# Performance work log

Measured on AMD Instinct MI355X. Metric: run time of the kernel, lower is better.

## Reference

```python
import jax, jax.numpy as jnp
import numpy as np

C = 64  # num_channels
B, H, W = 16, 160, 160


def squeeze2d(x, f=2):
    b, c, h, w = x.shape
    x = x.reshape(b, c, h // f, f, w // f, f)
    x = x.transpose(0, 1, 3, 5, 2, 4)
    return x.reshape(b, c * f * f, h // f, w // f)


def unsqueeze2d(x, f=2):
    b, c, h, w = x.shape
    x = x.reshape(b, c // (f * f), f, f, h, w)
    x = x.transpose(0, 1, 4, 2, 5, 3)
    return x.reshape(b, c // (f * f), h * f, w * f)


def get_indices(num_channels):
    # generate_ind(p) tiles the row-major-flattened 2x2 pattern over C//4 channel groups
    def gen(p):
        return np.tile(np.array(p, dtype=bool), num_channels // 4)
    m = np.ones(num_channels, dtype=bool)
    t = gen([0, 0, 1, 1]); b = ~t
    l = gen([0, 1, 0, 1]); r = ~l
    return (m, t, b, l, r, t & l, t & r, b & l, b & r)


INDS = get_indices(C)


def conv1x1(z, w):
    # 1x1 conv == channel matmul
    return jnp.einsum('oc,bchw->bohw', w, z)


def partition_input(x):
    z = unsqueeze2d(x)
    z = jnp.pad(z, ((0, 0), (0, 0), (1, 1), (1, 1)), constant_values=-1.0)
    z = squeeze2d(z)  # (B, C, H+1, W+1)
    m, t, b, l, r, tl, tr, bl, br = INDS
    return (z[:, :, 1:-1, 1:-1],
            z[:, t, :1, 1:-1], z[:, b, -1:, 1:-1],
            z[:, l, 1:-1, :1], z[:, r, 1:-1, -1:],
            z[:, tl, :1, :1], z[:, tr, :1, -1:],
            z[:, bl, -1:, :1], z[:, br, -1:, -1:])


def unsqueeze_line(ze):
    b, c = ze.shape[:2]
    sz = (1, -1) if ze.shape[-2] == 1 else (-1, 1)
    return ze.reshape(b, c // 2, 2, -1).transpose(0, 1, 3, 2).reshape(b, c // 2, *sz)


def merge_output(z_m, z_t, z_b, z_l, z_r, z_tl, z_tr, z_bl, z_br):
    z_m = unsqueeze2d(z_m)
    z_t, z_b, z_l, z_r = [unsqueeze_line(zi) for zi in (z_t, z_b, z_l, z_r)]
    z_tt = jnp.concatenate([z_tl, z_t, z_tr], axis=3)
    z_mm = jnp.concatenate([z_l, z_m, z_r], axis=3)
    z_bb = jnp.concatenate([z_bl, z_b, z_br], axis=3)
    return squeeze2d(jnp.concatenate([z_tt, z_mm, z_bb], axis=2))


def setup_inputs() -> dict:
    key = jax.random.key(0)
    k1, k2 = jax.random.split(key)
    x = jax.random.normal(k1, (B, C, H, W), dtype=jnp.float32)
    logdet = jax.random.normal(k2, (B,), dtype=jnp.float32)
    rng = np.random.RandomState(0)
    w_init = np.linalg.qr(rng.randn(C, C))[0].astype(np.float32)
    weight = jnp.asarray(w_init)
    return {"input": x, "logdet": logdet, "weight": weight}


def reference(input, logdet, weight):
    h, w = input.shape[-2:]
    pixels = [(h - 1) * (w - 1), w - 1, w - 1, h - 1, h - 1, 1, 1, 1, 1]
    ws = [weight[np.ix_(ind, ind)] for ind in INDS]
    dlogdet = sum(jnp.linalg.slogdet(wi)[1] * p for wi, p in zip(ws, pixels))
    zs = partition_input(input)
    outs = [conv1x1(z, wi) for z, wi in zip(zs, ws)]
    output = merge_output(*outs)
    return output, logdet + dlogdet
```

## Files before the change

kernel.cpp:

```cpp
#include <hip/hip_runtime.h>
#include <math.h>

#define NB 16
#define NC 64
#define HW 160
#define PLANE (HW * HW)
#define SG 161
#define SGSQ (SG * SG)
#define NSITES (NB * SGSQ)
#define OUT_LD_OFF (NB * NC * PLANE)
#define TILE 256
#define NCONV ((NSITES + TILE - 1) / TILE)

#define SMEM_FLOATS 9476

__device__ inline int chmap(int i, int n, int pa, int pb) {
    if (n == 64) return i;
    if (n == 32) return ((i >> 1) << 2) | ((i & 1) ? pb : pa);
    return (i << 2) | pa;
}

template <int N>
__device__ float group_lu_logabsdet(const float* __restrict__ W, float* A,
                                    int pa, int pb, int lane) {
    const int r = lane & (N - 1);
    constexpr int LD = N + 1;
#pragma unroll 4
    for (int i = 0; i < N; ++i)
        A[i * LD + r] = W[chmap(i, N, pa, pb) * 64 + chmap(r, N, pa, pb)];
    asm volatile("s_waitcnt lgkmcnt(0) vmcnt(0)" ::: "memory");
    float logdet = 0.f;
    for (int k = 0; k < N; ++k) {
        float cand = (r >= k) ? fabsf(A[r * LD + k]) : -1.f;
        int idx = r;
#pragma unroll
        for (int off = N >> 1; off; off >>= 1) {
            float oc = __shfl_xor(cand, off, N);
            int oi = __shfl_xor(idx, off, N);
            if (oc > cand || (oc == cand && oi < idx)) { cand = oc; idx = oi; }
        }
        const int p = idx;
        if (p != k) {
            float tk = A[k * LD + r];
            float tp = A[p * LD + r];
            A[k * LD + r] = tp;
            A[p * LD + r] = tk;
        }
        asm volatile("s_waitcnt lgkmcnt(0)" ::: "memory");
        float piv = A[k * LD + k];
        logdet += logf(fabsf(piv));
        float rpiv = 1.f / piv;
        if (r > k) {
            float wk = A[k * LD + r] * rpiv;
            int i = k + 1;
            for (; i + 3 < N; i += 4) {
                float a0 = A[(i + 0) * LD + k], a1 = A[(i + 1) * LD + k],
                      a2 = A[(i + 2) * LD + k], a3 = A[(i + 3) * LD + k];
                float x0 = A[(i + 0) * LD + r], x1 = A[(i + 1) * LD + r],
                      x2 = A[(i + 2) * LD + r], x3 = A[(i + 3) * LD + r];
                A[(i + 0) * LD + r] = fmaf(-a0, wk, x0);
                A[(i + 1) * LD + r] = fmaf(-a1, wk, x1);
                A[(i + 2) * LD + r] = fmaf(-a2, wk, x2);
                A[(i + 3) * LD + r] = fmaf(-a3, wk, x3);
            }
            for (; i < N; ++i) {
                float a0 = A[i * LD + k], x0 = A[i * LD + r];
                A[i * LD + r] = fmaf(-a0, wk, x0);
            }
        }
        asm volatile("s_waitcnt lgkmcnt(0)" ::: "memory");
    }
    return logdet;
}

__global__ __launch_bounds__(256, 4) void InvConv1x1GridAlign_kernel(
    const float* __restrict__ x, const float* __restrict__ ld_in,
    const float* __restrict__ W, float* __restrict__ out) {
    __shared__ __align__(16) float smem[SMEM_FLOATS];
    const int tid = threadIdx.x;

    if (blockIdx.x == 0) {
        float* A64 = smem;
        float* A32a = smem + 4160;
        float* A32b = smem + 6272;
        float* A16 = smem + 8384;
        float* partial = smem + 9472;
        int wid = tid >> 6;
        int lane = tid & 63;
        float part = 0.f;
        if (wid == 0) {
            part = 25281.f * group_lu_logabsdet<64>(W, A64, 0, 0, lane);
        } else if (wid == 1) {
            int g = lane >> 5;
            float ld = group_lu_logabsdet<32>(W, A32a + g * (32 * 33),
                                              g ? 0 : 2, g ? 1 : 3, lane);
            part = (__shfl(ld, 0, 64) + __shfl(ld, 32, 64)) * 159.f;
        } else if (wid == 2) {
            int g = lane >> 5;
            float ld = group_lu_logabsdet<32>(W, A32b + g * (32 * 33),
                                              g ? 0 : 1, g ? 2 : 3, lane);
            part = (__shfl(ld, 0, 64) + __shfl(ld, 32, 64)) * 159.f;
        } else {
            int g = lane >> 4;
            float ld = group_lu_logabsdet<16>(W, A16 + g * (16 * 17),
                                              3 - g, 0, lane);
            part = __shfl(ld, 0, 64) + __shfl(ld, 16, 64) +
                   __shfl(ld, 32, 64) + __shfl(ld, 48, 64);
        }
        if (lane == 0) partial[wid] = part;
        __syncthreads();
        if (tid < NB) {
            float dl = partial[0] + partial[1] + partial[2] + partial[3];
            out[OUT_LD_OFF + tid] = ld_in[tid] + dl;
        }
        return;
    }

    const int tile0 = ((int)blockIdx.x - 1) * TILE;
    const int lane = tid & 63;
    const int wid = tid >> 6;
    const int wo = __builtin_amdgcn_readfirstlane(wid << 4);

    const int offm[4] = {0, 1, HW, HW + 1};
    bool vm[4];
    int baseoff;
    const float* xb;
    {
        int s = tile0 + tid;
        bool sok = s < NSITES;
        unsigned us = (unsigned)(sok ? s : 0);
        unsigned b = us / SGSQ;
        unsigned rr = us - b * SGSQ;
        unsigned Y = rr / SG;
        unsigned X = rr - Y * SG;
        xb = x + (size_t)b * (NC * PLANE);
        baseoff = ((int)Y - 1) * HW + ((int)X - 1);
        bool okT = sok && (Y >= 1), okB = sok && (Y <= HW - 1);
        bool okL = (X >= 1), okR = (X <= HW - 1);
        vm[0] = okT && okL; vm[1] = okT && okR;
        vm[2] = okB && okL; vm[3] = okB && okR;
    }

    float acc[16][4];
#pragma unroll
    for (int j = 0; j < 16; ++j)
#pragma unroll
        for (int s2 = 0; s2 < 4; ++s2) acc[j][s2] = 0.f;

#pragma unroll 1
    for (int half = 0; half < 2; ++half) {
        __syncthreads();
#pragma unroll 8
        for (int krow = 0; krow < 32; ++krow) {
            const int k = (half << 5) + krow;
            const int pl = k ^ 3;
            const int m = krow & 3;
            float val = vm[m] ? xb[pl * PLANE + baseoff + offm[m]] : 0.f;
            smem[(krow << 8) + tid] = val;
        }
        __syncthreads();
#pragma unroll 1
        for (int kb = 0; kb < 8; ++kb) {
            float v[4][4];
            const float* vb = smem + (kb << 10) + lane;
#pragma unroll
            for (int kk = 0; kk < 4; ++kk)
#pragma unroll
                for (int s2 = 0; s2 < 4; ++s2)
                    v[kk][s2] = vb[(kk << 8) + (s2 << 6)];
            const int k0 = (half << 5) + (kb << 2);
#pragma unroll
            for (int jb = 0; jb < 2; ++jb) {
                float4 w4[8];
#pragma unroll
                for (int j = 0; j < 8; ++j)
                    w4[j] = *(const float4*)(W + (wo + (jb << 3) + j) * 64 + k0);
#pragma unroll
                for (int j = 0; j < 8; ++j) {
                    const int jj = (jb << 3) + j;
#pragma unroll
                    for (int kk = 0; kk < 4; ++kk) {
                        const float wjk = (kk == 0) ? w4[j].x
                                        : (kk == 1) ? w4[j].y
                                        : (kk == 2) ? w4[j].z : w4[j].w;
#pragma unroll
                        for (int s2 = 0; s2 < 4; ++s2)
                            acc[jj][s2] = fmaf(wjk, v[kk][s2], acc[jj][s2]);
                    }
                }
            }
        }
    }

#pragma unroll
    for (int s2 = 0; s2 < 4; ++s2) {
        int s = tile0 + lane + (s2 << 6);
        bool sok = s < NSITES;
        unsigned us = (unsigned)(sok ? s : 0);
        unsigned b = us / SGSQ;
        unsigned rr = us - b * SGSQ;
        unsigned Y = rr / SG;
        unsigned X = rr - Y * SG;
        float* ob = out + (size_t)b * (NC * PLANE);
        int boff = ((int)Y - 1) * HW + ((int)X - 1);
        bool okT = sok && (Y >= 1), okB = sok && (Y <= HW - 1);
        bool okL = (X >= 1), okR = (X <= HW - 1);
        bool wm[4] = {okT && okL, okT && okR, okB && okL, okB && okR};
#pragma unroll
        for (int j = 0; j < 16; ++j) {
            const int o = wo + j;
            const int pl = o ^ 3;
            const int m = j & 3;
            if (wm[m]) ob[pl * PLANE + boff + offm[m]] = acc[j][s2];
        }
    }
}

extern "C" void kernel_launch(void* const* d_in, const int* in_sizes, int n_in,
                              void* d_out, int out_size, void* d_ws, size_t ws_size,
                              hipStream_t stream) {
    const float* x = (const float*)d_in[0];
    const float* ld = (const float*)d_in[1];
    const float* W = (const float*)d_in[2];
    float* out = (float*)d_out;
    hipLaunchKernelGGL(InvConv1x1GridAlign_kernel, dim3(NCONV + 1), dim3(256), 0,
                       stream, x, ld, W, out);
}
```

Measured before the change: 252.5 us.

## Split determinant into separate kernel and register-tile conv without shared memory

Moves the LU log-determinant work into its own single-block kernel launched after the main conv kernel. The main kernel now has each thread own one site and compute 32 of the 64 output channels, using two blocks per tile. Inputs are loaded straight from global memory into registers with double-buffered 16-channel chunks and masked by multiplication instead of staged through LDS. This drops shared memory and barriers, but each input is now read twice (once per output half), there is a second launch, and register pressure rises.

```diff
diff --git a/kernel.cpp b/kernel.cpp
--- a/kernel.cpp
+++ b/kernel.cpp
@@ -12,7 +12,7 @@
 #define TILE 256
 #define NCONV ((NSITES + TILE - 1) / TILE)
 
-#define SMEM_FLOATS 9476
+#define DET_SMEM_FLOATS 9476
 
 __device__ inline int chmap(int i, int n, int pa, int pb) {
     if (n == 64) return i;
@@ -73,60 +73,91 @@
     return logdet;
 }
 
-__global__ __launch_bounds__(256, 4) void InvConv1x1GridAlign_kernel(
-    const float* __restrict__ x, const float* __restrict__ ld_in,
-    const float* __restrict__ W, float* __restrict__ out) {
-    __shared__ __align__(16) float smem[SMEM_FLOATS];
+__global__ __launch_bounds__(256, 4) void InvConvDet_kernel(
+    const float* __restrict__ ld_in, const float* __restrict__ W,
+    float* __restrict__ out) {
+    __shared__ __align__(16) float smem[DET_SMEM_FLOATS];
     const int tid = threadIdx.x;
-
-    if (blockIdx.x == 0) {
-        float* A64 = smem;
-        float* A32a = smem + 4160;
-        float* A32b = smem + 6272;
-        float* A16 = smem + 8384;
-        float* partial = smem + 9472;
-        int wid = tid >> 6;
-        int lane = tid & 63;
-        float part = 0.f;
-        if (wid == 0) {
-            part = 25281.f * group_lu_logabsdet<64>(W, A64, 0, 0, lane);
-        } else if (wid == 1) {
-            int g = lane >> 5;
-            float ld = group_lu_logabsdet<32>(W, A32a + g * (32 * 33),
-                                              g ? 0 : 2, g ? 1 : 3, lane);
-            part = (__shfl(ld, 0, 64) + __shfl(ld, 32, 64)) * 159.f;
-        } else if (wid == 2) {
-            int g = lane >> 5;
-            float ld = group_lu_logabsdet<32>(W, A32b + g * (32 * 33),
-                                              g ? 0 : 1, g ? 2 : 3, lane);
-            part = (__shfl(ld, 0, 64) + __shfl(ld, 32, 64)) * 159.f;
-        } else {
-            int g = lane >> 4;
-            float ld = group_lu_logabsdet<16>(W, A16 + g * (16 * 17),
-                                              3 - g, 0, lane);
-            part = __shfl(ld, 0, 64) + __shfl(ld, 16, 64) +
-                   __shfl(ld, 32, 64) + __shfl(ld, 48, 64);
-        }
-        if (lane == 0) partial[wid] = part;
-        __syncthreads();
-        if (tid < NB) {
-            float dl = partial[0] + partial[1] + partial[2] + partial[3];
-            out[OUT_LD_OFF + tid] = ld_in[tid] + dl;
-        }
-        return;
-    }
-
-    const int tile0 = ((int)blockIdx.x - 1) * TILE;
-    const int lane = tid & 63;
-    const int wid = tid >> 6;
-    const int wo = __builtin_amdgcn_readfirstlane(wid << 4);
+    float* A64 = smem;
+    float* A32a = smem + 4160;
+    float* A32b = smem + 6272;
+    float* A16 = smem + 8384;
+    float* partial = smem + 9472;
+    int wid = tid >> 6;
+    int lane = tid & 63;
+    float part = 0.f;
+    if (wid == 0) {
+        part = 25281.f * group_lu_logabsdet<64>(W, A64, 0, 0, lane);
+    } else if (wid == 1) {
+        int g = lane >> 5;
+        float ld = group_lu_logabsdet<32>(W, A32a + g * (32 * 33),
+                                          g ? 0 : 2, g ? 1 : 3, lane);
+        part = (__shfl(ld, 0, 64) + __shfl(ld, 32, 64)) * 159.f;
+    } else if (wid == 2) {
+        int g = lane >> 5;
+        float ld = group_lu_logabsdet<32>(W, A32b + g * (32 * 33),
+                                          g ? 0 : 1, g ? 2 : 3, lane);
+        part = (__shfl(ld, 0, 64) + __shfl(ld, 32, 64)) * 159.f;
+    } else {
+        int g = lane >> 4;
+        float ld = group_lu_logabsdet<16>(W, A16 + g * (16 * 17), 3 - g, 0, lane);
+        part = __shfl(ld, 0, 64) + __shfl(ld, 16, 64) +
+               __shfl(ld, 32, 64) + __shfl(ld, 48, 64);
+    }
+    if (lane == 0) partial[wid] = part;
+    __syncthreads();
+    if (tid < NB) {
+        float dl = partial[0] + partial[1] + partial[2] + partial[3];
+        out[OUT_LD_OFF + tid] = ld_in[tid] + dl;
+    }
+}
+
+
+#define LOADCH(dst, cc)                                                      \
+    {                                                                        \
+        _Pragma("unroll") for (int i = 0; i < 16; ++i)                       \
+            dst[i] = xb[(size_t)(((cc) << 4) + (i ^ 3)) * PLANE +            \
+                        aoff[i & 3]];                                        \
+    }
+
+#define COMPCH(src, cc)                                                      \
+    {                                                                        \
+        _Pragma("unroll") for (int i = 0; i < 16; ++i) src[i] *= mf[i & 3];  \
+        _Pragma("unroll") for (int j = 0; j < 32; ++j) {                     \
+            const float* wr = wbase + j * 64 + ((cc) << 4);                  \
+            float4 w0 = *(const float4*)(wr + 0);                            \
+            float4 w1 = *(const float4*)(wr + 4);                            \
+            float4 w2 = *(const float4*)(wr + 8);                            \
+            float4 w3 = *(const float4*)(wr + 12);                           \
+            float a = u[j];                                                  \
+            a = fmaf(w0.x, src[0], a);  a = fmaf(w0.y, src[1], a);           \
+            a = fmaf(w0.z, src[2], a);  a = fmaf(w0.w, src[3], a);           \
+            a = fmaf(w1.x, src[4], a);  a = fmaf(w1.y, src[5], a);           \
+            a = fmaf(w1.z, src[6], a);  a = fmaf(w1.w, src[7], a);           \
+            a = fmaf(w2.x, src[8], a);  a = fmaf(w2.y, src[9], a);           \
+            a = fmaf(w2.z, src[10], a); a = fmaf(w2.w, src[11], a);          \
+            a = fmaf(w3.x, src[12], a); a = fmaf(w3.y, src[13], a);          \
+            a = fmaf(w3.z, src[14], a); a = fmaf(w3.w, src[15], a);          \
+            u[j] = a;                                                        \
+        }                                                                    \
+    }
+
+__global__ __launch_bounds__(256, 5) void InvConvMain_kernel(
+    const float* __restrict__ x, const float* __restrict__ W,
+    float* __restrict__ out) {
+    const int tid = threadIdx.x;
+    const int bid = blockIdx.x;
+    const int ohalf = bid & 1;
+    const int s = (bid >> 1) * TILE + tid;
 
     const int offm[4] = {0, 1, HW, HW + 1};
     bool vm[4];
+    int aoff[4];
+    float mf[4];
     int baseoff;
     const float* xb;
+    float* ob;
     {
-        int s = tile0 + tid;
         bool sok = s < NSITES;
         unsigned us = (unsigned)(sok ? s : 0);
         unsigned b = us / SGSQ;
@@ -134,84 +165,44 @@
         unsigned Y = rr / SG;
         unsigned X = rr - Y * SG;
         xb = x + (size_t)b * (NC * PLANE);
+        ob = out + (size_t)b * (NC * PLANE);
         baseoff = ((int)Y - 1) * HW + ((int)X - 1);
         bool okT = sok && (Y >= 1), okB = sok && (Y <= HW - 1);
         bool okL = (X >= 1), okR = (X <= HW - 1);
         vm[0] = okT && okL; vm[1] = okT && okR;
         vm[2] = okB && okL; vm[3] = okB && okR;
-    }
-
-    float acc[16][4];
-#pragma unroll
-    for (int j = 0; j < 16; ++j)
-#pragma unroll
-        for (int s2 = 0; s2 < 4; ++s2) acc[j][s2] = 0.f;
-
-#pragma unroll 1
-    for (int half = 0; half < 2; ++half) {
-        __syncthreads();
-#pragma unroll 8
-        for (int krow = 0; krow < 32; ++krow) {
-            const int k = (half << 5) + krow;
-            const int pl = k ^ 3;
-            const int m = krow & 3;
-            float val = vm[m] ? xb[pl * PLANE + baseoff + offm[m]] : 0.f;
-            smem[(krow << 8) + tid] = val;
-        }
-        __syncthreads();
-#pragma unroll 1
-        for (int kb = 0; kb < 8; ++kb) {
-            float v[4][4];
-            const float* vb = smem + (kb << 10) + lane;
-#pragma unroll
-            for (int kk = 0; kk < 4; ++kk)
-#pragma unroll
-                for (int s2 = 0; s2 < 4; ++s2)
-                    v[kk][s2] = vb[(kk << 8) + (s2 << 6)];
-            const int k0 = (half << 5) + (kb << 2);
-#pragma unroll
-            for (int jb = 0; jb < 2; ++jb) {
-                float4 w4[8];
-#pragma unroll
-                for (int j = 0; j < 8; ++j)
-                    w4[j] = *(const float4*)(W + (wo + (jb << 3) + j) * 64 + k0);
-#pragma unroll
-                for (int j = 0; j < 8; ++j) {
-                    const int jj = (jb << 3) + j;
-#pragma unroll
-                    for (int kk = 0; kk < 4; ++kk) {
-                        const float wjk = (kk == 0) ? w4[j].x
-                                        : (kk == 1) ? w4[j].y
-                                        : (kk == 2) ? w4[j].z : w4[j].w;
-#pragma unroll
-                        for (int s2 = 0; s2 < 4; ++s2)
-                            acc[jj][s2] = fmaf(wjk, v[kk][s2], acc[jj][s2]);
-                    }
-                }
+#pragma unroll
+        for (int m = 0; m < 4; ++m) {
+            aoff[m] = vm[m] ? (baseoff + offm[m]) : 0;
+            mf[m] = vm[m] ? 1.f : 0.f;
+        }
+    }
+
+    const float* wbase = W + (ohalf << 5) * 64;
+
+    float u[32];
+#pragma unroll
+    for (int j = 0; j < 32; ++j) u[j] = 0.f;
+
+    float va[16], vb[16];
+    LOADCH(va, 0)
+    LOADCH(vb, 1)
+    COMPCH(va, 0)
+    LOADCH(va, 2)
+    COMPCH(vb, 1)
+    LOADCH(vb, 3)
+    COMPCH(va, 2)
+    COMPCH(vb, 3)
+
+#pragma unroll
+    for (int m = 0; m < 4; ++m) {
+        if (vm[m]) {
+#pragma unroll
+            for (int t = 0; t < 8; ++t) {
+                int j = (t << 2) + m;
+                ob[(size_t)((ohalf << 5) + (j ^ 3)) * PLANE + baseoff +
+                   offm[m]] = u[j];
             }
-        }
-    }
-
-#pragma unroll
-    for (int s2 = 0; s2 < 4; ++s2) {
-        int s = tile0 + lane + (s2 << 6);
-        bool sok = s < NSITES;
-        unsigned us = (unsigned)(sok ? s : 0);
-        unsigned b = us / SGSQ;
-        unsigned rr = us - b * SGSQ;
-        unsigned Y = rr / SG;
-        unsigned X = rr - Y * SG;
-        float* ob = out + (size_t)b * (NC * PLANE);
-        int boff = ((int)Y - 1) * HW + ((int)X - 1);
-        bool okT = sok && (Y >= 1), okB = sok && (Y <= HW - 1);
-        bool okL = (X >= 1), okR = (X <= HW - 1);
-        bool wm[4] = {okT && okL, okT && okR, okB && okL, okB && okR};
-#pragma unroll
-        for (int j = 0; j < 16; ++j) {
-            const int o = wo + j;
-            const int pl = o ^ 3;
-            const int m = j & 3;
-            if (wm[m]) ob[pl * PLANE + boff + offm[m]] = acc[j][s2];
         }
     }
 }
@@ -223,6 +214,8 @@
     const float* ld = (const float*)d_in[1];
     const float* W = (const float*)d_in[2];
     float* out = (float*)d_out;
-    hipLaunchKernelGGL(InvConv1x1GridAlign_kernel, dim3(NCONV + 1), dim3(256), 0,
-                       stream, x, ld, W, out);
-}
+    hipLaunchKernelGGL(InvConvMain_kernel, dim3(2 * NCONV), dim3(256), 0,
+                       stream, x, W, out);
+    hipLaunchKernelGGL(InvConvDet_kernel, dim3(1), dim3(256), 0,
+                       stream, ld, W, out);
+}
```

After: 308.1 us. +22.0%, slower.
